# Performance work log

Hardware: AMD Instinct MI355X
Metric: run time of the kernel (lower is better)

Reference implementation:

```python
import jax, jax.numpy as jnp
import numpy as np

B, N, E, F = 8, 16384, 64, 64


def euler_zyx_to_matrix(J):
    # J: [..., 3] euler angles (alpha about Z, beta about Y, gamma about X)
    # R = Rz(alpha) @ Ry(beta) @ Rx(gamma)  (pytorch3d 'ZYX' convention)
    a, b, g = J[..., 0], J[..., 1], J[..., 2]
    ca, sa = jnp.cos(a), jnp.sin(a)
    cb, sb = jnp.cos(b), jnp.sin(b)
    cg, sg = jnp.cos(g), jnp.sin(g)
    r00 = ca * cb
    r01 = ca * sb * sg - sa * cg
    r02 = ca * sb * cg + sa * sg
    r10 = sa * cb
    r11 = sa * sb * sg + ca * cg
    r12 = sa * sb * cg - ca * sg
    r20 = -sb
    r21 = cb * sg
    r22 = cb * cg
    R = jnp.stack([
        jnp.stack([r00, r01, r02], axis=-1),
        jnp.stack([r10, r11, r12], axis=-1),
        jnp.stack([r20, r21, r22], axis=-1),
    ], axis=-2)  # [..., 3, 3]
    return R


def setup_inputs() -> dict:
    key = jax.random.key(0)
    k1, k2, k3, k4, k5 = jax.random.split(key, 5)
    X = jax.random.normal(k1, (B, N, E, 3), dtype=jnp.float32)
    J = jax.random.uniform(k2, (B, N, E, 3), dtype=jnp.float32)
    A = jax.random.normal(k3, (F, E), dtype=jnp.float32)
    Bw = jax.random.normal(k4, (F, E), dtype=jnp.float32)
    C = jax.random.normal(k5, (F, E), dtype=jnp.float32)
    return {"X": X, "J": J, "A": A, "Bw": Bw, "C": C}


def reference(X, J, A, Bw, C):
    R = euler_zyx_to_matrix(J)                 # [B, N, E, 3, 3]
    # v = R^T X  (per-point 3-vector): v_i = sum_k R[..., k, i] * X[..., k]
    v = jnp.einsum('bneki,bnek->bnei', R, X)   # [B, N, E, 3]
    col0 = R[..., :, 0]                        # [B, N, E, 3]
    col1 = R[..., :, 1]
    col2 = R[..., :, 2]
    v0 = v[..., 0:1]
    v1 = v[..., 1:2]
    v2 = v[..., 2:3]
    a_term = col0 * v0 + col1 * v1             # [B, N, E, 3]
    b_term = col1 * v0 - col0 * v1
    c_term = col2 * v2
    Y = (jnp.einsum('fe,bnei->bnfi', A, a_term)
         + jnp.einsum('fe,bnei->bnfi', Bw, b_term)
         + jnp.einsum('fe,bnei->bnfi', C, c_term))
    return Y
```

## Files before the change

### kernel.cpp

```cpp
#include <hip/hip_runtime.h>


#define NPOS   131072
#define PB     16
#define NC     (PB * 3)
#define ITERS  8
#define BLOCKS 1024
#define THREADS 256
#define PPW    4

typedef _Float16 half8 __attribute__((ext_vector_type(8)));
typedef float floatx4 __attribute__((ext_vector_type(4)));

__global__ __launch_bounds__(THREADS, 4)
void fused_mfma(const float* __restrict__ X, const float* __restrict__ J,
                const float* __restrict__ A, const float* __restrict__ Bw,
                const float* __restrict__ Cm, float* __restrict__ Y) {
    __shared__ _Float16 Tl[2][6][NC][4][8];

    const int lane = threadIdx.x & 63;
    const int w    = threadIdx.x >> 6;

    const int fa  = w * 16 + (lane & 15);
    const int kgA = lane >> 4;
    half8 afrag[6];
    #pragma unroll
    for (int ks = 0; ks < 6; ++ks) {
        const float* mat = (ks < 2) ? A : (ks < 4 ? Bw : Cm);
        const float* src = mat + fa * 64 + (ks & 1) * 32 + kgA * 8;
        float4 lo = *(const float4*)src;
        float4 hi = *(const float4*)(src + 4);
        half8 h;
        h[0] = (_Float16)lo.x; h[1] = (_Float16)lo.y;
        h[2] = (_Float16)lo.z; h[3] = (_Float16)lo.w;
        h[4] = (_Float16)hi.x; h[5] = (_Float16)hi.y;
        h[6] = (_Float16)hi.z; h[7] = (_Float16)hi.w;
        afrag[ks] = h;
    }

    const int ks0 = lane >> 5;
    const int kgW = (lane & 31) >> 3;
    const int jW  = lane & 7;

    float jr[PPW][3], xr[PPW][3];

    auto LOAD = [&](int it) {
        #pragma unroll
        for (int q = 0; q < PPW; ++q) {
            const int p = (blockIdx.x * ITERS + it) * PB + w * PPW + q;
            const float* jp = J + (size_t)(p * 64 + lane) * 3;
            const float* xp = X + (size_t)(p * 64 + lane) * 3;
            jr[q][0] = jp[0]; jr[q][1] = jp[1]; jr[q][2] = jp[2];
            xr[q][0] = xp[0]; xr[q][1] = xp[1]; xr[q][2] = xp[2];
        }
    };

    auto P1 = [&](int buf) {
        #pragma unroll
        for (int q = 0; q < PPW; ++q) {
            const int p_local = w * PPW + q;
            float ja = jr[q][0], jb = jr[q][1], jg = jr[q][2];
            float x0 = xr[q][0], x1 = xr[q][1], x2 = xr[q][2];
            float sa, ca, sb, cb, sg, cg;
            __sincosf(ja, &sa, &ca);
            __sincosf(jb, &sb, &cb);
            __sincosf(jg, &sg, &cg);
            float casb = ca * sb, sasb = sa * sb;
            float r00 = ca * cb, r01 = casb * sg - sa * cg, r02 = casb * cg + sa * sg;
            float r10 = sa * cb, r11 = sasb * sg + ca * cg, r12 = sasb * cg - ca * sg;
            float r20 = -sb,     r21 = cb * sg,             r22 = cb * cg;
            float v0 = fmaf(r00, x0, fmaf(r10, x1, r20 * x2));
            float v1 = fmaf(r01, x0, fmaf(r11, x1, r21 * x2));
            float v2 = fmaf(r02, x0, fmaf(r12, x1, r22 * x2));
            float a0 = fmaf(r00, v0, r01 * v1);
            float a1 = fmaf(r10, v0, r11 * v1);
            float a2 = fmaf(r20, v0, r21 * v1);
            float b0 = fmaf(r01, v0, -r00 * v1);
            float b1 = fmaf(r11, v0, -r10 * v1);
            float b2 = fmaf(r21, v0, -r20 * v1);
            float c0 = r02 * v2, c1 = r12 * v2, c2 = r22 * v2;

            const int n0 = p_local * 3;
            Tl[buf][0 + ks0][n0 + 0][kgW][jW] = (_Float16)a0;
            Tl[buf][0 + ks0][n0 + 1][kgW][jW] = (_Float16)a1;
            Tl[buf][0 + ks0][n0 + 2][kgW][jW] = (_Float16)a2;
            Tl[buf][2 + ks0][n0 + 0][kgW][jW] = (_Float16)b0;
            Tl[buf][2 + ks0][n0 + 1][kgW][jW] = (_Float16)b1;
            Tl[buf][2 + ks0][n0 + 2][kgW][jW] = (_Float16)b2;
            Tl[buf][4 + ks0][n0 + 0][kgW][jW] = (_Float16)c0;
            Tl[buf][4 + ks0][n0 + 1][kgW][jW] = (_Float16)c1;
            Tl[buf][4 + ks0][n0 + 2][kgW][jW] = (_Float16)c2;
        }
    };

    auto P2 = [&](int it, int buf) {
        #pragma unroll
        for (int nt = 0; nt < 3; ++nt) {
            floatx4 acc = {0.f, 0.f, 0.f, 0.f};
            #pragma unroll
            for (int ks = 0; ks < 6; ++ks) {
                half8 b = *(const half8*)&Tl[buf][ks][nt * 16 + (lane & 15)][lane >> 4][0];
                acc = __builtin_amdgcn_mfma_f32_16x16x32_f16(afrag[ks], b, acc, 0, 0, 0);
            }
            const int n = nt * 16 + (lane & 15);
            const int pl2 = (n * 171) >> 9;
            const int i2  = n - pl2 * 3;
            const int p2  = (blockIdx.x * ITERS + it) * PB + pl2;
            float* yp = Y + (size_t)p2 * 192 + i2;
            const int fbase = w * 16 + (lane >> 4) * 4;
            #pragma unroll
            for (int r = 0; r < 4; ++r)
                __builtin_nontemporal_store(acc[r], &yp[(fbase + r) * 3]);
        }
    };

    LOAD(0);
    P1(0);
    for (int t = 0; t < ITERS; ++t) {
        __syncthreads();
        if (t + 1 < ITERS) LOAD(t + 1);
        P2(t, t & 1);
        if (t + 1 < ITERS) P1((t + 1) & 1);
    }
}

extern "C" void kernel_launch(void* const* d_in, const int* in_sizes, int n_in,
                              void* d_out, int out_size, void* d_ws, size_t ws_size,
                              hipStream_t stream) {
    const float* X  = (const float*)d_in[0];
    const float* J  = (const float*)d_in[1];
    const float* A  = (const float*)d_in[2];
    const float* Bw = (const float*)d_in[3];
    const float* Cm = (const float*)d_in[4];
    float* Y = (float*)d_out;
    fused_mfma<<<BLOCKS, THREADS, 0, stream>>>(X, J, A, Bw, Cm, Y);
}
```

Measured before the change: 65.60 us.

## Single-buffer LDS tile with XOR swizzle, more blocks and higher occupancy

Drops the LDS double buffer in favor of a single buffer, which needs a second barrier between the MFMA read phase and the next write phase. Adds an XOR swizzle on the k-group index for both writes and reads to cut LDS bank conflicts. Doubles the block count, halves iterations per block, and raises the launch-bounds occupancy hint to 8 blocks per CU. The extra barrier gives up some of the overlap between compute and the next tile's writes, and the tighter register budget may cause spills.

```diff
diff --git a/kernel.cpp b/kernel.cpp
--- a/kernel.cpp
+++ b/kernel.cpp
@@ -4,19 +4,19 @@
 #define NPOS   131072
 #define PB     16
 #define NC     (PB * 3)
-#define ITERS  8
-#define BLOCKS 1024
+#define ITERS  4
+#define BLOCKS 2048
 #define THREADS 256
 #define PPW    4
 
 typedef _Float16 half8 __attribute__((ext_vector_type(8)));
 typedef float floatx4 __attribute__((ext_vector_type(4)));
 
-__global__ __launch_bounds__(THREADS, 4)
+__global__ __launch_bounds__(THREADS, 8)
 void fused_mfma(const float* __restrict__ X, const float* __restrict__ J,
                 const float* __restrict__ A, const float* __restrict__ Bw,
                 const float* __restrict__ Cm, float* __restrict__ Y) {
-    __shared__ _Float16 Tl[2][6][NC][4][8];
+    __shared__ _Float16 Tl[6][NC][4][8];
 
     const int lane = threadIdx.x & 63;
     const int w    = threadIdx.x >> 6;
@@ -41,6 +41,7 @@
     const int ks0 = lane >> 5;
     const int kgW = (lane & 31) >> 3;
     const int jW  = lane & 7;
+    const int kgR = (lane >> 4) ^ (((lane & 15) >> 1) & 3);
 
     float jr[PPW][3], xr[PPW][3];
 
@@ -55,7 +56,7 @@
         }
     };
 
-    auto P1 = [&](int buf) {
+    auto P1 = [&]() {
         #pragma unroll
         for (int q = 0; q < PPW; ++q) {
             const int p_local = w * PPW + q;
@@ -72,34 +73,33 @@
             float v0 = fmaf(r00, x0, fmaf(r10, x1, r20 * x2));
             float v1 = fmaf(r01, x0, fmaf(r11, x1, r21 * x2));
             float v2 = fmaf(r02, x0, fmaf(r12, x1, r22 * x2));
-            float a0 = fmaf(r00, v0, r01 * v1);
-            float a1 = fmaf(r10, v0, r11 * v1);
-            float a2 = fmaf(r20, v0, r21 * v1);
-            float b0 = fmaf(r01, v0, -r00 * v1);
-            float b1 = fmaf(r11, v0, -r10 * v1);
-            float b2 = fmaf(r21, v0, -r20 * v1);
-            float c0 = r02 * v2, c1 = r12 * v2, c2 = r22 * v2;
+            float ta[3], tb[3], tc[3];
+            ta[0] = fmaf(r00, v0, r01 * v1);
+            ta[1] = fmaf(r10, v0, r11 * v1);
+            ta[2] = fmaf(r20, v0, r21 * v1);
+            tb[0] = fmaf(r01, v0, -r00 * v1);
+            tb[1] = fmaf(r11, v0, -r10 * v1);
+            tb[2] = fmaf(r21, v0, -r20 * v1);
+            tc[0] = r02 * v2; tc[1] = r12 * v2; tc[2] = r22 * v2;
 
-            const int n0 = p_local * 3;
-            Tl[buf][0 + ks0][n0 + 0][kgW][jW] = (_Float16)a0;
-            Tl[buf][0 + ks0][n0 + 1][kgW][jW] = (_Float16)a1;
-            Tl[buf][0 + ks0][n0 + 2][kgW][jW] = (_Float16)a2;
-            Tl[buf][2 + ks0][n0 + 0][kgW][jW] = (_Float16)b0;
-            Tl[buf][2 + ks0][n0 + 1][kgW][jW] = (_Float16)b1;
-            Tl[buf][2 + ks0][n0 + 2][kgW][jW] = (_Float16)b2;
-            Tl[buf][4 + ks0][n0 + 0][kgW][jW] = (_Float16)c0;
-            Tl[buf][4 + ks0][n0 + 1][kgW][jW] = (_Float16)c1;
-            Tl[buf][4 + ks0][n0 + 2][kgW][jW] = (_Float16)c2;
+            #pragma unroll
+            for (int i = 0; i < 3; ++i) {
+                const int n  = p_local * 3 + i;
+                const int kg = kgW ^ ((n >> 1) & 3);
+                Tl[0 + ks0][n][kg][jW] = (_Float16)ta[i];
+                Tl[2 + ks0][n][kg][jW] = (_Float16)tb[i];
+                Tl[4 + ks0][n][kg][jW] = (_Float16)tc[i];
+            }
         }
     };
 
-    auto P2 = [&](int it, int buf) {
+    auto P2 = [&](int it) {
         #pragma unroll
         for (int nt = 0; nt < 3; ++nt) {
             floatx4 acc = {0.f, 0.f, 0.f, 0.f};
             #pragma unroll
             for (int ks = 0; ks < 6; ++ks) {
-                half8 b = *(const half8*)&Tl[buf][ks][nt * 16 + (lane & 15)][lane >> 4][0];
+                half8 b = *(const half8*)&Tl[ks][nt * 16 + (lane & 15)][kgR][0];
                 acc = __builtin_amdgcn_mfma_f32_16x16x32_f16(afrag[ks], b, acc, 0, 0, 0);
             }
             const int n = nt * 16 + (lane & 15);
@@ -115,12 +115,15 @@
     };
 
     LOAD(0);
-    P1(0);
+    P1();
     for (int t = 0; t < ITERS; ++t) {
         __syncthreads();
         if (t + 1 < ITERS) LOAD(t + 1);
-        P2(t, t & 1);
-        if (t + 1 < ITERS) P1((t + 1) & 1);
+        P2(t);
+        if (t + 1 < ITERS) {
+            __syncthreads();
+            P1();
+        }
     }
 }
 
```

New measurement: 163.4 us. +149.0%, slower.
